# Kernel optimization log

Measured on AMD Instinct MI355X. Metric: run time of the kernel, lower is better.

## Reference

```python
import jax, jax.numpy as jnp
import numpy as np

N = 20000      # tuple-graph nodes
E = 320000     # edges per relation
F_IN = 5189    # 80 one-hot + 3*1703 node features
DIM = 256
N_ORIG = 183   # original texas graph nodes
C = 7


def _gcn(x, W, b, src, dst, n):
    # PyG GCNConv: add self loops, symmetric deg^-1/2 normalization, aggregate src->dst.
    loop = jnp.arange(n)
    s = jnp.concatenate([src, loop])
    d = jnp.concatenate([dst, loop])
    deg = jax.ops.segment_sum(jnp.ones(s.shape[0], x.dtype), d, num_segments=n)
    dinv = jnp.where(deg > 0, jax.lax.rsqrt(deg), 0.0)
    norm = dinv[s] * dinv[d]            # [E+n]
    h = x @ W                            # [n, dim]
    out = jax.ops.segment_sum(h[s] * norm[:, None], d, num_segments=n)
    return out + b


def _mlp(h, w1, b1, w2, b2):
    return jnp.maximum(h @ w1 + b1, 0.0) @ w2 + b2


def _seg_mean(h, idx, n):
    s = jax.ops.segment_sum(h, idx, num_segments=n)
    cnt = jax.ops.segment_sum(jnp.ones(idx.shape[0], h.dtype), idx, num_segments=n)
    return s / jnp.maximum(cnt, 1.0)[:, None]


def setup_inputs() -> dict:
    key = jax.random.key(0)
    ks = jax.random.split(key, 16)
    sc_in = 1.0 / np.sqrt(F_IN)
    sc_d = 1.0 / np.sqrt(DIM)
    sc_3d = 1.0 / np.sqrt(3 * DIM)
    inp = {
        'x': jax.random.normal(ks[0], (N, F_IN), jnp.float32),
        'w1': jax.random.normal(ks[1], (3, F_IN, DIM), jnp.float32) * sc_in,
        'b1': jnp.zeros((3, DIM), jnp.float32),
        'w2': jax.random.normal(ks[2], (3, DIM, DIM), jnp.float32) * sc_d,
        'b2': jnp.zeros((3, DIM), jnp.float32),
        'm1w1': jax.random.normal(ks[3], (3 * DIM, DIM), jnp.float32) * sc_3d,
        'm1b1': jnp.zeros((DIM,), jnp.float32),
        'm1w2': jax.random.normal(ks[4], (DIM, DIM), jnp.float32) * sc_d,
        'm1b2': jnp.zeros((DIM,), jnp.float32),
        'm2w1': jax.random.normal(ks[5], (3 * DIM, DIM), jnp.float32) * sc_3d,
        'm2b1': jnp.zeros((DIM,), jnp.float32),
        'm2w2': jax.random.normal(ks[6], (DIM, DIM), jnp.float32) * sc_d,
        'm2b2': jnp.zeros((DIM,), jnp.float32),
        'mw1': jax.random.normal(ks[7], (3 * DIM, DIM), jnp.float32) * sc_3d,
        'mb1': jnp.zeros((DIM,), jnp.float32),
        'mw2': jax.random.normal(ks[8], (DIM, C), jnp.float32) * sc_d,
        'mb2': jnp.zeros((C,), jnp.float32),
        'edge_index_1': jax.random.randint(ks[9], (2, E), 0, N),
        'edge_index_2': jax.random.randint(ks[10], (2, E), 0, N),
        'edge_index_3': jax.random.randint(ks[11], (2, E), 0, N),
        'index_1': jax.random.randint(ks[12], (N,), 0, N_ORIG),
        'index_2': jax.random.randint(ks[13], (N,), 0, N_ORIG),
        'index_3': jax.random.randint(ks[14], (N,), 0, N_ORIG),
    }
    return inp


def reference(x, w1, b1, w2, b2, m1w1, m1b1, m1w2, m1b2,
              m2w1, m2b1, m2w2, m2b2, mw1, mb1, mw2, mb2,
              edge_index_1, edge_index_2, edge_index_3,
              index_1, index_2, index_3):
    n = x.shape[0]
    eis = (edge_index_1, edge_index_2, edge_index_3)
    # layer 1: three GCN convs over the three relations, ReLU, concat, MLP
    hs = [jnp.maximum(_gcn(x, w1[i], b1[i], eis[i][0], eis[i][1], n), 0.0) for i in range(3)]
    h = _mlp(jnp.concatenate(hs, axis=-1), m1w1, m1b1, m1w2, m1b2)
    # layer 2
    hs = [jnp.maximum(_gcn(h, w2[i], b2[i], eis[i][0], eis[i][1], n), 0.0) for i in range(3)]
    h = _mlp(jnp.concatenate(hs, axis=-1), m2w1, m2b1, m2w2, m2b2)
    # faithful to source bug: index_2 is overwritten by index_3 before scatter
    x1 = _seg_mean(h, index_1, N_ORIG)
    x2 = _seg_mean(h, index_3, N_ORIG)
    x3 = _seg_mean(h, index_3, N_ORIG)
    out = _mlp(jnp.concatenate([x1, x2, x3], axis=1), mw1, mb1, mw2, mb2)
    return jax.nn.log_softmax(out, axis=1)
```

## Files before the change

### kernel.cpp

```cpp
#include <hip/hip_runtime.h>
#include <hip/hip_bf16.h>
#include <cstdint>
#include <cstddef>

typedef __bf16 bf16_t;
typedef __bf16 bf16x8 __attribute__((ext_vector_type(8)));
typedef float f32x4 __attribute__((ext_vector_type(4)));
typedef unsigned int u32x4 __attribute__((ext_vector_type(4)));

#define NN 20000
#define NE 320000
#define FIN 5189
#define KP1 5216
#define NORIG 183

__device__ inline f32x4 ld4u(const float* p) {
  f32x4 v; __builtin_memcpy(&v, p, 16); return v;
}

__device__ inline void gload_lds16(const bf16_t* g, bf16_t* l) {
  __builtin_amdgcn_global_load_lds(
      (const __attribute__((address_space(1))) uint32_t*)g,
      (__attribute__((address_space(3))) uint32_t*)l, 16, 0, 0);
}

__global__ void k_cvtpad(const float* __restrict__ x, bf16_t* __restrict__ xb) {
  const int total = NN * (KP1 / 8);
  for (int idx = blockIdx.x * 256 + threadIdx.x; idx < total; idx += gridDim.x * 256) {
    int row = idx / (KP1 / 8);
    int c8  = idx - row * (KP1 / 8);
    int col = c8 * 8;
    bf16x8 v{};
    const float* xp = x + (size_t)row * FIN + col;
    if (col + 8 <= FIN) {
      f32x4 a = ld4u(xp), b = ld4u(xp + 4);
#pragma unroll
      for (int j = 0; j < 4; ++j) { v[j] = (bf16_t)a[j]; v[4 + j] = (bf16_t)b[j]; }
    } else {
#pragma unroll
      for (int j = 0; j < 8; ++j) v[j] = (col + j < FIN) ? (bf16_t)xp[j] : (bf16_t)0.f;
    }
    *(bf16x8*)&xb[(size_t)row * KP1 + col] = v;
  }
}

#define BM1 128
#define BN1 256
#define NT1 (KP1 / 32)

__global__ __launch_bounds__(512) void k_gemm1(
    const bf16_t* __restrict__ A, const bf16_t* __restrict__ Bt,
    float* __restrict__ C, int M)
{
  __shared__ __align__(16) bf16_t As[2][BM1 * 32];
  __shared__ __align__(16) bf16_t Bs[2][BN1 * 32];
  const int tid = threadIdx.x, lane = tid & 63, wave = tid >> 6;
  const int m0 = blockIdx.y * BM1, n0 = blockIdx.x * BN1;
  const int wr = (wave >> 2) * 64, wc = (wave & 3) * 64;
  const int fm = lane & 15, fs = lane >> 4;

  const int arow = tid >> 2, asl = tid & 3;
  const int aks = asl ^ ((arow ^ (arow >> 2)) & 3);
  int agrow = m0 + arow; if (agrow >= M) agrow = M - 1;
  const bf16_t* asrc = A + (size_t)agrow * KP1 + aks * 8;

  const int br0 = tid >> 2;
  const int br1 = 128 + (tid >> 2);
  const int bks0 = asl ^ ((br0 ^ (br0 >> 2)) & 3);
  const int bks1 = asl ^ ((br1 ^ (br1 >> 2)) & 3);
  const bf16_t* bsrc0 = Bt + (size_t)(n0 + br0) * KP1 + bks0 * 8;
  const bf16_t* bsrc1 = Bt + (size_t)(n0 + br1) * KP1 + bks1 * 8;

  bf16_t* adst  = &As[0][0] + wave * 512;
  bf16_t* bdst0 = &Bs[0][0] + wave * 512;
  bf16_t* bdst1 = &Bs[0][0] + 4096 + wave * 512;

  int aoff[4], boff[4];
#pragma unroll
  for (int i = 0; i < 4; ++i) {
    int ra = wr + i * 16 + fm;
    aoff[i] = ra * 32 + ((fs ^ ((ra ^ (ra >> 2)) & 3)) * 8);
    int rb = wc + i * 16 + fm;
    boff[i] = rb * 32 + ((fs ^ ((rb ^ (rb >> 2)) & 3)) * 8);
  }

  f32x4 acc[4][4];
#pragma unroll
  for (int i = 0; i < 4; ++i)
#pragma unroll
    for (int j = 0; j < 4; ++j) acc[i][j] = {0.f, 0.f, 0.f, 0.f};

#define STAGE1(buf, kof) do { \
    gload_lds16(asrc + (kof),  adst  + (buf) * (BM1 * 32)); \
    gload_lds16(bsrc0 + (kof), bdst0 + (buf) * (BN1 * 32)); \
    gload_lds16(bsrc1 + (kof), bdst1 + (buf) * (BN1 * 32)); \
  } while (0)

  STAGE1(0, 0);
  __syncthreads();

  int buf = 0;
  for (int t = 0; t < NT1 - 1; ++t) {
    STAGE1(buf ^ 1, (t + 1) * 32);
    bf16x8 af[4], bfv[4];
#pragma unroll
    for (int i = 0; i < 4; ++i) af[i] = *(const bf16x8*)&As[buf][aoff[i]];
#pragma unroll
    for (int j = 0; j < 4; ++j) bfv[j] = *(const bf16x8*)&Bs[buf][boff[j]];
#pragma unroll
    for (int i = 0; i < 4; ++i)
#pragma unroll
      for (int j = 0; j < 4; ++j)
        acc[i][j] = __builtin_amdgcn_mfma_f32_16x16x32_bf16(af[i], bfv[j], acc[i][j], 0, 0, 0);
    __syncthreads();
    buf ^= 1;
  }
  {
    bf16x8 af[4], bfv[4];
#pragma unroll
    for (int i = 0; i < 4; ++i) af[i] = *(const bf16x8*)&As[buf][aoff[i]];
#pragma unroll
    for (int j = 0; j < 4; ++j) bfv[j] = *(const bf16x8*)&Bs[buf][boff[j]];
#pragma unroll
    for (int i = 0; i < 4; ++i)
#pragma unroll
      for (int j = 0; j < 4; ++j)
        acc[i][j] = __builtin_amdgcn_mfma_f32_16x16x32_bf16(af[i], bfv[j], acc[i][j], 0, 0, 0);
  }

  const int ccol = n0 + wc + fm;
#pragma unroll
  for (int i = 0; i < 4; ++i) {
    const int rb2 = m0 + wr + i * 16 + (lane >> 4) * 4;
#pragma unroll
    for (int r = 0; r < 4; ++r) {
      const int row = rb2 + r;
      if (row < M) {
        float* cp = C + (size_t)row * 768 + ccol;
#pragma unroll
        for (int j = 0; j < 4; ++j) cp[j * 16] = acc[i][j][r];
      }
    }
  }
}

#define BM 128
#define BN 128
#define BK 32
#define PADK 40

__global__ __launch_bounds__(256) void k_gemm(
    const float* __restrict__ A, const bf16_t* __restrict__ Bt,
    float* __restrict__ C, const float* __restrict__ bias,
    int M, int N, int K, int Kp, int relu)
{
  __shared__ __align__(16) bf16_t As[BM * PADK];
  __shared__ __align__(16) bf16_t Bs[BN * PADK];
  const int tid  = threadIdx.x;
  const int lane = tid & 63, wave = tid >> 6;
  const int m0 = blockIdx.y * BM, n0 = blockIdx.x * BN;
  const int wr = (wave >> 1) * 64, wc = (wave & 1) * 64;
  const int srow = tid >> 1;
  const int skh  = (tid & 1) * 16;
  const int arow = m0 + srow;
  const int fm = lane & 15;
  const int fk = (lane >> 4) * 8;

  f32x4 acc[4][4];
#pragma unroll
  for (int i = 0; i < 4; ++i)
#pragma unroll
    for (int j = 0; j < 4; ++j) acc[i][j] = {0.f, 0.f, 0.f, 0.f};

  for (int k0 = 0; k0 < Kp; k0 += BK) {
    {
      bf16x8 v0{}, v1{};
      if (arow < M) {
        const int kb = k0 + skh;
        const float* ap = A + (size_t)arow * K + kb;
        if (kb + 16 <= K) {
          f32x4 a = ld4u(ap), b = ld4u(ap + 4), c = ld4u(ap + 8), d = ld4u(ap + 12);
#pragma unroll
          for (int j = 0; j < 4; ++j) {
            v0[j]     = (bf16_t)a[j];
            v0[4 + j] = (bf16_t)b[j];
            v1[j]     = (bf16_t)c[j];
            v1[4 + j] = (bf16_t)d[j];
          }
        } else {
#pragma unroll
          for (int j = 0; j < 8; ++j) {
            int k1 = kb + j, k2 = kb + 8 + j;
            v0[j] = (bf16_t)((k1 < K) ? ap[j] : 0.f);
            v1[j] = (bf16_t)((k2 < K) ? ap[8 + j] : 0.f);
          }
        }
      }
      *(bf16x8*)&As[srow * PADK + skh]     = v0;
      *(bf16x8*)&As[srow * PADK + skh + 8] = v1;
    }
    {
      const bf16_t* bp = Bt + (size_t)(n0 + srow) * Kp + k0 + skh;
      u32x4 b0 = *(const u32x4*)bp;
      u32x4 b1 = *(const u32x4*)(bp + 8);
      *(u32x4*)&Bs[srow * PADK + skh]     = b0;
      *(u32x4*)&Bs[srow * PADK + skh + 8] = b1;
    }
    __syncthreads();

    bf16x8 af[4], bfv[4];
#pragma unroll
    for (int i = 0; i < 4; ++i) af[i] = *(const bf16x8*)&As[(wr + i * 16 + fm) * PADK + fk];
#pragma unroll
    for (int j = 0; j < 4; ++j) bfv[j] = *(const bf16x8*)&Bs[(wc + j * 16 + fm) * PADK + fk];
#pragma unroll
    for (int i = 0; i < 4; ++i)
#pragma unroll
      for (int j = 0; j < 4; ++j)
        acc[i][j] = __builtin_amdgcn_mfma_f32_16x16x32_bf16(af[i], bfv[j], acc[i][j], 0, 0, 0);
    __syncthreads();
  }

  const int ccol = n0 + wc + fm;
#pragma unroll
  for (int i = 0; i < 4; ++i) {
    const int rb = m0 + wr + i * 16 + (lane >> 4) * 4;
#pragma unroll
    for (int r = 0; r < 4; ++r) {
      const int row = rb + r;
      if (row < M) {
        float* cp = C + (size_t)row * N + ccol;
#pragma unroll
        for (int j = 0; j < 4; ++j) {
          float v = acc[i][j][r];
          if (bias) v += bias[ccol + j * 16];
          if (relu) v = fmaxf(v, 0.f);
          cp[j * 16] = v;
        }
      }
    }
  }
}

__global__ void k_transw(const float* __restrict__ src, bf16_t* __restrict__ dst,
                         int K, int Kp)
{
  __shared__ float tile[32][33];
  const int g = blockIdx.z;
  const int k0 = blockIdx.x * 32, j0 = blockIdx.y * 32;
  const int tx = threadIdx.x, ty = threadIdx.y;
  const float* sp = src + (size_t)g * K * 256;
#pragma unroll
  for (int i = 0; i < 4; ++i) {
    int k = k0 + ty + i * 8;
    tile[ty + i * 8][tx] = (k < K) ? sp[(size_t)k * 256 + j0 + tx] : 0.f;
  }
  __syncthreads();
  bf16_t* dp = dst + (size_t)g * 256 * Kp;
#pragma unroll
  for (int i = 0; i < 4; ++i) {
    int n = j0 + ty + i * 8;
    dp[(size_t)n * Kp + k0 + tx] = (bf16_t)tile[tx][ty + i * 8];
  }
}

__global__ void k_deg(const int* __restrict__ dst, int* __restrict__ cnt, int E) {
  int e = blockIdx.x * 256 + threadIdx.x;
  if (e < E) atomicAdd(&cnt[dst[e]], 1);
}

__global__ void k_dinv(const int* __restrict__ deg, float* __restrict__ dinv) {
  int v = blockIdx.x * 256 + threadIdx.x;
  if (v < 3 * NN) dinv[v] = rsqrtf((float)(deg[v] + 1));
}

#define SCAN_T 1024
#define SCAN_CH 20
__global__ __launch_bounds__(SCAN_T) void k_scan(
    const int* __restrict__ deg, int* __restrict__ rp, int* __restrict__ cur)
{
  const int r = blockIdx.x;
  const int* d = deg + r * NN;
  int* rpr = rp + r * (NN + 1);
  int* cr  = cur + r * NN;
  __shared__ int ts[SCAN_T];
  const int t = threadIdx.x;
  const int base = t * SCAN_CH;
  int local[SCAN_CH];
  int sum = 0;
#pragma unroll
  for (int i = 0; i < SCAN_CH; ++i) {
    int v = base + i;
    int x = (v < NN) ? d[v] : 0;
    local[i] = sum; sum += x;
  }
  ts[t] = sum; __syncthreads();
  for (int ofs = 1; ofs < SCAN_T; ofs <<= 1) {
    int v = ts[t];
    int w = (t >= ofs) ? ts[t - ofs] : 0;
    __syncthreads();
    ts[t] = v + w;
    __syncthreads();
  }
  int excl = (t == 0) ? 0 : ts[t - 1];
#pragma unroll
  for (int i = 0; i < SCAN_CH; ++i) {
    int v = base + i;
    if (v < NN) { int val = excl + local[i]; rpr[v] = val; cr[v] = val; }
  }
  if (t == SCAN_T - 1) rpr[NN] = ts[SCAN_T - 1];
}

__global__ void k_bucket(const int* __restrict__ src, const int* __restrict__ dst,
                         int* __restrict__ cur, int* __restrict__ col) {
  int e = blockIdx.x * 256 + threadIdx.x;
  if (e < NE) {
    int d = dst[e];
    int pos = atomicAdd(&cur[d], 1);
    col[pos] = src[e];
  }
}

__global__ __launch_bounds__(256) void k_gather(
    const float* __restrict__ H, float* __restrict__ Out,
    const int* __restrict__ rp, const int* __restrict__ col,
    const float* __restrict__ dinv, const float* __restrict__ bias)
{
  const int v = blockIdx.x, r = blockIdx.y, tid = threadIdx.x;
  const int roff = r << 8;
  const int* rpr = rp + r * (NN + 1);
  const int* cr  = col + (size_t)r * NE;
  const float* dvp = dinv + r * NN;
  const float dv = dvp[v];
  float acc = H[(size_t)v * 768 + roff + tid] * dv;
  int i = rpr[v];
  const int e = rpr[v + 1];
  for (; i + 4 <= e; i += 4) {
    int s0 = cr[i], s1 = cr[i + 1], s2 = cr[i + 2], s3 = cr[i + 3];
    float d0 = dvp[s0], d1 = dvp[s1], d2 = dvp[s2], d3 = dvp[s3];
    float h0 = H[(size_t)s0 * 768 + roff + tid];
    float h1 = H[(size_t)s1 * 768 + roff + tid];
    float h2 = H[(size_t)s2 * 768 + roff + tid];
    float h3 = H[(size_t)s3 * 768 + roff + tid];
    acc += h0 * d0 + h1 * d1 + h2 * d2 + h3 * d3;
  }
  for (; i < e; ++i) {
    int s = cr[i];
    acc += H[(size_t)s * 768 + roff + tid] * dvp[s];
  }
  Out[(size_t)v * 768 + roff + tid] = fmaxf(dv * acc + bias[roff + tid], 0.f);
}

__global__ void k_segscatter(const float* __restrict__ h2,
                             const int* __restrict__ i1, const int* __restrict__ i3,
                             float* __restrict__ s1, float* __restrict__ s3,
                             float* __restrict__ c1, float* __restrict__ c3) {
  int v = blockIdx.x, c = threadIdx.x;
  float val = h2[(size_t)v * 256 + c];
  int g1 = i1[v], g3 = i3[v];
  atomicAdd(&s1[g1 * 256 + c], val);
  atomicAdd(&s3[g3 * 256 + c], val);
  if (c == 0) { atomicAdd(&c1[g1], 1.f); atomicAdd(&c3[g3], 1.f); }
}

__global__ __launch_bounds__(256) void k_final(
    const float* __restrict__ s1, const float* __restrict__ s3,
    const float* __restrict__ c1, const float* __restrict__ c3,
    const float* __restrict__ mw1, const float* __restrict__ mb1,
    const float* __restrict__ mw2, const float* __restrict__ mb2,
    float* __restrict__ out)
{
  __shared__ float xc[768];
  __shared__ float tt[256];
  __shared__ float lg[8];
  const int g = blockIdx.x, tid = threadIdx.x;
  float inv1 = 1.f / fmaxf(c1[g], 1.f);
  float inv3 = 1.f / fmaxf(c3[g], 1.f);
  float a3 = s3[g * 256 + tid] * inv3;
  xc[tid] = s1[g * 256 + tid] * inv1;
  xc[256 + tid] = a3;
  xc[512 + tid] = a3;
  __syncthreads();
  float acc = mb1[tid];
  for (int k = 0; k < 768; ++k) acc += xc[k] * mw1[k * 256 + tid];
  tt[tid] = fmaxf(acc, 0.f);
  __syncthreads();
  if (tid < 7) {
    float a = mb2[tid];
    for (int k = 0; k < 256; ++k) a += tt[k] * mw2[k * 7 + tid];
    lg[tid] = a;
  }
  __syncthreads();
  if (tid == 0) {
    float mx = lg[0];
    for (int c2 = 1; c2 < 7; ++c2) mx = fmaxf(mx, lg[c2]);
    float sum = 0.f;
    for (int c2 = 0; c2 < 7; ++c2) sum += expf(lg[c2] - mx);
    float lse = logf(sum) + mx;
    for (int c2 = 0; c2 < 7; ++c2) out[g * 7 + c2] = lg[c2] - lse;
  }
}

extern "C" void kernel_launch(void* const* d_in, const int* in_sizes, int n_in,
                              void* d_out, int out_size, void* d_ws, size_t ws_size,
                              hipStream_t stream) {
  const float* x    = (const float*)d_in[0];
  const float* w1   = (const float*)d_in[1];
  const float* b1   = (const float*)d_in[2];
  const float* w2   = (const float*)d_in[3];
  const float* b2   = (const float*)d_in[4];
  const float* m1w1 = (const float*)d_in[5];
  const float* m1b1 = (const float*)d_in[6];
  const float* m1w2 = (const float*)d_in[7];
  const float* m1b2 = (const float*)d_in[8];
  const float* m2w1 = (const float*)d_in[9];
  const float* m2b1 = (const float*)d_in[10];
  const float* m2w2 = (const float*)d_in[11];
  const float* m2b2 = (const float*)d_in[12];
  const float* mw1  = (const float*)d_in[13];
  const float* mb1  = (const float*)d_in[14];
  const float* mw2  = (const float*)d_in[15];
  const float* mb2  = (const float*)d_in[16];
  const int* e1 = (const int*)d_in[17];
  const int* e2 = (const int*)d_in[18];
  const int* e3 = (const int*)d_in[19];
  const int* i1 = (const int*)d_in[20];
  const int* i3 = (const int*)d_in[22];
  float* out = (float*)d_out;

  char* ws = (char*)d_ws;
  size_t off = 0;
  auto alloc = [&](size_t bytes) {
    char* p = ws + off;
    off += (bytes + 255) & ~(size_t)255;
    return (void*)p;
  };
  float*  buf1 = (float*)alloc((size_t)NN * 768 * 4);
  float*  buf2 = (float*)alloc((size_t)NN * 768 * 4);
  bf16_t* wt   = (bf16_t*)alloc((size_t)768 * KP1 * 2);
  int*    deg  = (int*)alloc((size_t)3 * NN * 4);
  float*  dinv = (float*)alloc((size_t)3 * NN * 4);
  int*    rp   = (int*)alloc((size_t)3 * (NN + 1) * 4);
  int*    cur  = (int*)alloc((size_t)3 * NN * 4);
  int*    col  = (int*)alloc((size_t)3 * NE * 4);
  float*  s1   = (float*)alloc((size_t)NORIG * 256 * 4);
  float*  s3   = (float*)alloc((size_t)NORIG * 256 * 4);
  float*  c1   = (float*)alloc((size_t)NORIG * 4);
  float*  c3   = (float*)alloc((size_t)NORIG * 4);
  bf16_t* xb   = (bf16_t*)alloc((size_t)NN * KP1 * 2);
  const bool fast1 = (off <= ws_size);

  hipMemsetAsync(deg, 0, (size_t)3 * NN * 4, stream);
  int gb = (NE + 255) / 256;
  k_deg<<<gb, 256, 0, stream>>>(e1 + NE, deg + 0 * NN, NE);
  k_deg<<<gb, 256, 0, stream>>>(e2 + NE, deg + 1 * NN, NE);
  k_deg<<<gb, 256, 0, stream>>>(e3 + NE, deg + 2 * NN, NE);
  k_dinv<<<(3 * NN + 255) / 256, 256, 0, stream>>>(deg, dinv);
  k_scan<<<3, SCAN_T, 0, stream>>>(deg, rp, cur);
  k_bucket<<<gb, 256, 0, stream>>>(e1, e1 + NE, cur + 0 * NN, col + 0 * (size_t)NE);
  k_bucket<<<gb, 256, 0, stream>>>(e2, e2 + NE, cur + 1 * NN, col + 1 * (size_t)NE);
  k_bucket<<<gb, 256, 0, stream>>>(e3, e3 + NE, cur + 2 * NN, col + 2 * (size_t)NE);

  auto gemm = [&](const float* A, const float* Wsrc, int G, float* C, const float* bias,
                  int M, int N, int K, int relu) {
    int Kp = (K + 31) & ~31;
    dim3 tg(Kp / 32, 8, G);
    k_transw<<<tg, dim3(32, 8), 0, stream>>>(Wsrc, wt, K, Kp);
    dim3 gg(N / 128, (M + 127) / 128);
    k_gemm<<<gg, 256, 0, stream>>>(A, wt, C, bias, M, N, K, Kp, relu);
  };

  dim3 gagg(NN, 3);

  if (fast1) {
    k_transw<<<dim3(KP1 / 32, 8, 3), dim3(32, 8), 0, stream>>>(w1, wt, FIN, KP1);
    k_cvtpad<<<2048, 256, 0, stream>>>(x, xb);
    k_gemm1<<<dim3(768 / BN1, (NN + BM1 - 1) / BM1), 512, 0, stream>>>(xb, wt, buf1, NN);
  } else {
    gemm(x, w1, 3, buf1, nullptr, NN, 768, FIN, 0);
  }
  k_gather<<<gagg, 256, 0, stream>>>(buf1, buf2, rp, col, dinv, b1);
  gemm(buf2, m1w1, 1, buf1, m1b1, NN, 256, 768, 1);
  gemm(buf1, m1w2, 1, buf2, m1b2, NN, 256, 256, 0);

  gemm(buf2, w2, 3, buf1, nullptr, NN, 768, 256, 0);
  k_gather<<<gagg, 256, 0, stream>>>(buf1, buf2, rp, col, dinv, b2);
  gemm(buf2, m2w1, 1, buf1, m2b1, NN, 256, 768, 1);
  gemm(buf1, m2w2, 1, buf2, m2b2, NN, 256, 256, 0);

  hipMemsetAsync(s1, 0, (size_t)NORIG * 256 * 4, stream);
  hipMemsetAsync(s3, 0, (size_t)NORIG * 256 * 4, stream);
  hipMemsetAsync(c1, 0, (size_t)NORIG * 4, stream);
  hipMemsetAsync(c3, 0, (size_t)NORIG * 4, stream);
  k_segscatter<<<NN, 256, 0, stream>>>(buf2, i1, i3, s1, s3, c1, c3);
  k_final<<<NORIG, 256, 0, stream>>>(s1, s3, c1, c3, mw1, mb1, mw2, mb2, out);
}
```

Baseline: 1.073 ms.

## Store intermediate activations in bf16 and use async-LDS GEMMs throughout

```diff
diff --git a/kernel.cpp b/kernel.cpp
--- a/kernel.cpp
+++ b/kernel.cpp
@@ -5,8 +5,8 @@
 
 typedef __bf16 bf16_t;
 typedef __bf16 bf16x8 __attribute__((ext_vector_type(8)));
+typedef __bf16 bf16x4 __attribute__((ext_vector_type(4)));
 typedef float f32x4 __attribute__((ext_vector_type(4)));
-typedef unsigned int u32x4 __attribute__((ext_vector_type(4)));
 
 #define NN 20000
 #define NE 320000
@@ -23,6 +23,8 @@
       (const __attribute__((address_space(1))) uint32_t*)g,
       (__attribute__((address_space(3))) uint32_t*)l, 16, 0, 0);
 }
+
+__device__ inline int swz(int r) { return (r ^ (r >> 2)) & 3; }
 
 __global__ void k_cvtpad(const float* __restrict__ x, bf16_t* __restrict__ xb) {
   const int total = NN * (KP1 / 8);
@@ -44,32 +46,26 @@
   }
 }
 
-#define BM1 128
-#define BN1 256
-#define NT1 (KP1 / 32)
-
-__global__ __launch_bounds__(512) void k_gemm1(
+__global__ __launch_bounds__(512) void k_gemm_w(
     const bf16_t* __restrict__ A, const bf16_t* __restrict__ Bt,
-    float* __restrict__ C, int M)
+    bf16_t* __restrict__ C, const float* __restrict__ bias,
+    int M, int N, int Kp, int relu)
 {
-  __shared__ __align__(16) bf16_t As[2][BM1 * 32];
-  __shared__ __align__(16) bf16_t Bs[2][BN1 * 32];
+  __shared__ __align__(16) bf16_t As[2][128 * 32];
+  __shared__ __align__(16) bf16_t Bs[2][256 * 32];
   const int tid = threadIdx.x, lane = tid & 63, wave = tid >> 6;
-  const int m0 = blockIdx.y * BM1, n0 = blockIdx.x * BN1;
+  const int m0 = blockIdx.y * 128, n0 = blockIdx.x * 256;
   const int wr = (wave >> 2) * 64, wc = (wave & 3) * 64;
   const int fm = lane & 15, fs = lane >> 4;
 
   const int arow = tid >> 2, asl = tid & 3;
-  const int aks = asl ^ ((arow ^ (arow >> 2)) & 3);
+  const int aks = asl ^ swz(arow);
   int agrow = m0 + arow; if (agrow >= M) agrow = M - 1;
-  const bf16_t* asrc = A + (size_t)agrow * KP1 + aks * 8;
-
-  const int br0 = tid >> 2;
-  const int br1 = 128 + (tid >> 2);
-  const int bks0 = asl ^ ((br0 ^ (br0 >> 2)) & 3);
-  const int bks1 = asl ^ ((br1 ^ (br1 >> 2)) & 3);
-  const bf16_t* bsrc0 = Bt + (size_t)(n0 + br0) * KP1 + bks0 * 8;
-  const bf16_t* bsrc1 = Bt + (size_t)(n0 + br1) * KP1 + bks1 * 8;
+  const bf16_t* asrc = A + (size_t)agrow * Kp + aks * 8;
+
+  const int br0 = tid >> 2, br1 = 128 + br0;
+  const bf16_t* bsrc0 = Bt + (size_t)(n0 + br0) * Kp + (asl ^ swz(br0)) * 8;
+  const bf16_t* bsrc1 = Bt + (size_t)(n0 + br1) * Kp + (asl ^ swz(br1)) * 8;
 
   bf16_t* adst  = &As[0][0] + wave * 512;
   bf16_t* bdst0 = &Bs[0][0] + wave * 512;
@@ -79,9 +75,9 @@
 #pragma unroll
   for (int i = 0; i < 4; ++i) {
     int ra = wr + i * 16 + fm;
-    aoff[i] = ra * 32 + ((fs ^ ((ra ^ (ra >> 2)) & 3)) * 8);
+    aoff[i] = ra * 32 + (fs ^ swz(ra)) * 8;
     int rb = wc + i * 16 + fm;
-    boff[i] = rb * 32 + ((fs ^ ((rb ^ (rb >> 2)) & 3)) * 8);
+    boff[i] = rb * 32 + (fs ^ swz(rb)) * 8;
   }
 
   f32x4 acc[4][4];
@@ -90,18 +86,18 @@
 #pragma unroll
     for (int j = 0; j < 4; ++j) acc[i][j] = {0.f, 0.f, 0.f, 0.f};
 
-#define STAGE1(buf, kof) do { \
-    gload_lds16(asrc + (kof),  adst  + (buf) * (BM1 * 32)); \
-    gload_lds16(bsrc0 + (kof), bdst0 + (buf) * (BN1 * 32)); \
-    gload_lds16(bsrc1 + (kof), bdst1 + (buf) * (BN1 * 32)); \
+#define STAGEW(buf, kof) do { \
+    gload_lds16(asrc + (kof),  adst  + (buf) * (128 * 32)); \
+    gload_lds16(bsrc0 + (kof), bdst0 + (buf) * (256 * 32)); \
+    gload_lds16(bsrc1 + (kof), bdst1 + (buf) * (256 * 32)); \
   } while (0)
 
-  STAGE1(0, 0);
+  const int NT = Kp / 32;
+  STAGEW(0, 0);
   __syncthreads();
-
   int buf = 0;
-  for (int t = 0; t < NT1 - 1; ++t) {
-    STAGE1(buf ^ 1, (t + 1) * 32);
+  for (int t = 0; t < NT - 1; ++t) {
+    STAGEW(buf ^ 1, (t + 1) * 32);
     bf16x8 af[4], bfv[4];
 #pragma unroll
     for (int i = 0; i < 4; ++i) af[i] = *(const bf16x8*)&As[buf][aoff[i]];
@@ -136,106 +132,113 @@
     for (int r = 0; r < 4; ++r) {
       const int row = rb2 + r;
       if (row < M) {
-        float* cp = C + (size_t)row * 768 + ccol;
-#pragma unroll
-        for (int j = 0; j < 4; ++j) cp[j * 16] = acc[i][j][r];
-      }
-    }
-  }
-}
-
-#define BM 128
-#define BN 128
-#define BK 32
-#define PADK 40
-
-__global__ __launch_bounds__(256) void k_gemm(
-    const float* __restrict__ A, const bf16_t* __restrict__ Bt,
-    float* __restrict__ C, const float* __restrict__ bias,
-    int M, int N, int K, int Kp, int relu)
-{
-  __shared__ __align__(16) bf16_t As[BM * PADK];
-  __shared__ __align__(16) bf16_t Bs[BN * PADK];
-  const int tid  = threadIdx.x;
-  const int lane = tid & 63, wave = tid >> 6;
-  const int m0 = blockIdx.y * BM, n0 = blockIdx.x * BN;
-  const int wr = (wave >> 1) * 64, wc = (wave & 1) * 64;
-  const int srow = tid >> 1;
-  const int skh  = (tid & 1) * 16;
-  const int arow = m0 + srow;
-  const int fm = lane & 15;
-  const int fk = (lane >> 4) * 8;
-
-  f32x4 acc[4][4];
-#pragma unroll
-  for (int i = 0; i < 4; ++i)
-#pragma unroll
-    for (int j = 0; j < 4; ++j) acc[i][j] = {0.f, 0.f, 0.f, 0.f};
-
-  for (int k0 = 0; k0 < Kp; k0 += BK) {
-    {
-      bf16x8 v0{}, v1{};
-      if (arow < M) {
-        const int kb = k0 + skh;
-        const float* ap = A + (size_t)arow * K + kb;
-        if (kb + 16 <= K) {
-          f32x4 a = ld4u(ap), b = ld4u(ap + 4), c = ld4u(ap + 8), d = ld4u(ap + 12);
-#pragma unroll
-          for (int j = 0; j < 4; ++j) {
-            v0[j]     = (bf16_t)a[j];
-            v0[4 + j] = (bf16_t)b[j];
-            v1[j]     = (bf16_t)c[j];
-            v1[4 + j] = (bf16_t)d[j];
-          }
-        } else {
-#pragma unroll
-          for (int j = 0; j < 8; ++j) {
-            int k1 = kb + j, k2 = kb + 8 + j;
-            v0[j] = (bf16_t)((k1 < K) ? ap[j] : 0.f);
-            v1[j] = (bf16_t)((k2 < K) ? ap[8 + j] : 0.f);
-          }
-        }
-      }
-      *(bf16x8*)&As[srow * PADK + skh]     = v0;
-      *(bf16x8*)&As[srow * PADK + skh + 8] = v1;
-    }
-    {
-      const bf16_t* bp = Bt + (size_t)(n0 + srow) * Kp + k0 + skh;
-      u32x4 b0 = *(const u32x4*)bp;
-      u32x4 b1 = *(const u32x4*)(bp + 8);
-      *(u32x4*)&Bs[srow * PADK + skh]     = b0;
-      *(u32x4*)&Bs[srow * PADK + skh + 8] = b1;
-    }
-    __syncthreads();
-
-    bf16x8 af[4], bfv[4];
-#pragma unroll
-    for (int i = 0; i < 4; ++i) af[i] = *(const bf16x8*)&As[(wr + i * 16 + fm) * PADK + fk];
-#pragma unroll
-    for (int j = 0; j < 4; ++j) bfv[j] = *(const bf16x8*)&Bs[(wc + j * 16 + fm) * PADK + fk];
-#pragma unroll
-    for (int i = 0; i < 4; ++i)
-#pragma unroll
-      for (int j = 0; j < 4; ++j)
-        acc[i][j] = __builtin_amdgcn_mfma_f32_16x16x32_bf16(af[i], bfv[j], acc[i][j], 0, 0, 0);
-    __syncthreads();
-  }
-
-  const int ccol = n0 + wc + fm;
-#pragma unroll
-  for (int i = 0; i < 4; ++i) {
-    const int rb = m0 + wr + i * 16 + (lane >> 4) * 4;
-#pragma unroll
-    for (int r = 0; r < 4; ++r) {
-      const int row = rb + r;
-      if (row < M) {
-        float* cp = C + (size_t)row * N + ccol;
+        bf16_t* cp = C + (size_t)row * N + ccol;
 #pragma unroll
         for (int j = 0; j < 4; ++j) {
           float v = acc[i][j][r];
           if (bias) v += bias[ccol + j * 16];
           if (relu) v = fmaxf(v, 0.f);
-          cp[j * 16] = v;
+          cp[j * 16] = (bf16_t)v;
+        }
+      }
+    }
+  }
+}
+
+__global__ __launch_bounds__(256) void k_gemm_s(
+    const bf16_t* __restrict__ A, const bf16_t* __restrict__ Bt,
+    bf16_t* __restrict__ C, const float* __restrict__ bias,
+    int M, int N, int Kp, int relu)
+{
+  __shared__ __align__(16) bf16_t As[2][128 * 32];
+  __shared__ __align__(16) bf16_t Bs[2][128 * 32];
+  const int tid = threadIdx.x, lane = tid & 63, wave = tid >> 6;
+  const int m0 = blockIdx.y * 128, n0 = blockIdx.x * 128;
+  const int wr = (wave >> 1) * 64, wc = (wave & 1) * 64;
+  const int fm = lane & 15, fs = lane >> 4;
+
+  const int r0 = tid >> 2, r1 = 64 + r0, sl = tid & 3;
+  int ag0 = m0 + r0; if (ag0 >= M) ag0 = M - 1;
+  int ag1 = m0 + r1; if (ag1 >= M) ag1 = M - 1;
+  const bf16_t* asrc0 = A + (size_t)ag0 * Kp + (sl ^ swz(r0)) * 8;
+  const bf16_t* asrc1 = A + (size_t)ag1 * Kp + (sl ^ swz(r1)) * 8;
+  const bf16_t* bsrc0 = Bt + (size_t)(n0 + r0) * Kp + (sl ^ swz(r0)) * 8;
+  const bf16_t* bsrc1 = Bt + (size_t)(n0 + r1) * Kp + (sl ^ swz(r1)) * 8;
+
+  bf16_t* adst0 = &As[0][0] + wave * 512;
+  bf16_t* adst1 = &As[0][0] + 2048 + wave * 512;
+  bf16_t* bdst0 = &Bs[0][0] + wave * 512;
+  bf16_t* bdst1 = &Bs[0][0] + 2048 + wave * 512;
+
+  int aoff[4], boff[4];
+#pragma unroll
+  for (int i = 0; i < 4; ++i) {
+    int ra = wr + i * 16 + fm;
+    aoff[i] = ra * 32 + (fs ^ swz(ra)) * 8;
+    int rb = wc + i * 16 + fm;
+    boff[i] = rb * 32 + (fs ^ swz(rb)) * 8;
+  }
+
+  f32x4 acc[4][4];
+#pragma unroll
+  for (int i = 0; i < 4; ++i)
+#pragma unroll
+    for (int j = 0; j < 4; ++j) acc[i][j] = {0.f, 0.f, 0.f, 0.f};
+
+#define STAGES(buf, kof) do { \
+    gload_lds16(asrc0 + (kof), adst0 + (buf) * (128 * 32)); \
+    gload_lds16(asrc1 + (kof), adst1 + (buf) * (128 * 32)); \
+    gload_lds16(bsrc0 + (kof), bdst0 + (buf) * (128 * 32)); \
+    gload_lds16(bsrc1 + (kof), bdst1 + (buf) * (128 * 32)); \
+  } while (0)
+
+  const int NT = Kp / 32;
+  STAGES(0, 0);
+  __syncthreads();
+  int buf = 0;
+  for (int t = 0; t < NT - 1; ++t) {
+    STAGES(buf ^ 1, (t + 1) * 32);
+    bf16x8 af[4], bfv[4];
+#pragma unroll
+    for (int i = 0; i < 4; ++i) af[i] = *(const bf16x8*)&As[buf][aoff[i]];
+#pragma unroll
+    for (int j = 0; j < 4; ++j) bfv[j] = *(const bf16x8*)&Bs[buf][boff[j]];
+#pragma unroll
+    for (int i = 0; i < 4; ++i)
+#pragma unroll
+      for (int j = 0; j < 4; ++j)
+        acc[i][j] = __builtin_amdgcn_mfma_f32_16x16x32_bf16(af[i], bfv[j], acc[i][j], 0, 0, 0);
+    __syncthreads();
+    buf ^= 1;
+  }
+  {
+    bf16x8 af[4], bfv[4];
+#pragma unroll
+    for (int i = 0; i < 4; ++i) af[i] = *(const bf16x8*)&As[buf][aoff[i]];
+#pragma unroll
+    for (int j = 0; j < 4; ++j) bfv[j] = *(const bf16x8*)&Bs[buf][boff[j]];
+#pragma unroll
+    for (int i = 0; i < 4; ++i)
+#pragma unroll
+      for (int j = 0; j < 4; ++j)
+        acc[i][j] = __builtin_amdgcn_mfma_f32_16x16x32_bf16(af[i], bfv[j], acc[i][j], 0, 0, 0);
+  }
+
+  const int ccol = n0 + wc + fm;
+#pragma unroll
+  for (int i = 0; i < 4; ++i) {
+    const int rb2 = m0 + wr + i * 16 + (lane >> 4) * 4;
+#pragma unroll
+    for (int r = 0; r < 4; ++r) {
+      const int row = rb2 + r;
+      if (row < M) {
+        bf16_t* cp = C + (size_t)row * N + ccol;
+#pragma unroll
+        for (int j = 0; j < 4; ++j) {
+          float v = acc[i][j][r];
+          if (bias) v += bias[ccol + j * 16];
+          if (relu) v = fmaxf(v, 0.f);
+          cp[j * 16] = (bf16_t)v;
         }
       }
     }
@@ -321,42 +324,59 @@
   }
 }
 
-__global__ __launch_bounds__(256) void k_gather(
-    const float* __restrict__ H, float* __restrict__ Out,
+__global__ __launch_bounds__(256) void k_gatherb(
+    const bf16_t* __restrict__ H, bf16_t* __restrict__ Out,
     const int* __restrict__ rp, const int* __restrict__ col,
     const float* __restrict__ dinv, const float* __restrict__ bias)
 {
-  const int v = blockIdx.x, r = blockIdx.y, tid = threadIdx.x;
+  const int wv = threadIdx.x >> 6, lane = threadIdx.x & 63;
+  const int v = blockIdx.x * 4 + wv;
+  const int r = blockIdx.y;
   const int roff = r << 8;
   const int* rpr = rp + r * (NN + 1);
   const int* cr  = col + (size_t)r * NE;
   const float* dvp = dinv + r * NN;
   const float dv = dvp[v];
-  float acc = H[(size_t)v * 768 + roff + tid] * dv;
+  const int c0 = roff + lane * 4;
+
+  bf16x4 hs = *(const bf16x4*)&H[(size_t)v * 768 + c0];
+  float a0 = (float)hs[0] * dv, a1 = (float)hs[1] * dv,
+        a2 = (float)hs[2] * dv, a3 = (float)hs[3] * dv;
+
   int i = rpr[v];
   const int e = rpr[v + 1];
-  for (; i + 4 <= e; i += 4) {
-    int s0 = cr[i], s1 = cr[i + 1], s2 = cr[i + 2], s3 = cr[i + 3];
-    float d0 = dvp[s0], d1 = dvp[s1], d2 = dvp[s2], d3 = dvp[s3];
-    float h0 = H[(size_t)s0 * 768 + roff + tid];
-    float h1 = H[(size_t)s1 * 768 + roff + tid];
-    float h2 = H[(size_t)s2 * 768 + roff + tid];
-    float h3 = H[(size_t)s3 * 768 + roff + tid];
-    acc += h0 * d0 + h1 * d1 + h2 * d2 + h3 * d3;
-  }
-  for (; i < e; ++i) {
+  for (; i + 2 <= e; i += 2) {
+    int s0 = cr[i], s1 = cr[i + 1];
+    float d0 = dvp[s0], d1 = dvp[s1];
+    bf16x4 h0 = *(const bf16x4*)&H[(size_t)s0 * 768 + c0];
+    bf16x4 h1 = *(const bf16x4*)&H[(size_t)s1 * 768 + c0];
+    a0 += (float)h0[0] * d0 + (float)h1[0] * d1;
+    a1 += (float)h0[1] * d0 + (float)h1[1] * d1;
+    a2 += (float)h0[2] * d0 + (float)h1[2] * d1;
+    a3 += (float)h0[3] * d0 + (float)h1[3] * d1;
+  }
+  if (i < e) {
     int s = cr[i];
-    acc += H[(size_t)s * 768 + roff + tid] * dvp[s];
-  }
-  Out[(size_t)v * 768 + roff + tid] = fmaxf(dv * acc + bias[roff + tid], 0.f);
-}
-
-__global__ void k_segscatter(const float* __restrict__ h2,
+    float d = dvp[s];
+    bf16x4 h = *(const bf16x4*)&H[(size_t)s * 768 + c0];
+    a0 += (float)h[0] * d; a1 += (float)h[1] * d;
+    a2 += (float)h[2] * d; a3 += (float)h[3] * d;
+  }
+  f32x4 bb = ld4u(bias + c0);
+  bf16x4 o;
+  o[0] = (bf16_t)fmaxf(dv * a0 + bb[0], 0.f);
+  o[1] = (bf16_t)fmaxf(dv * a1 + bb[1], 0.f);
+  o[2] = (bf16_t)fmaxf(dv * a2 + bb[2], 0.f);
+  o[3] = (bf16_t)fmaxf(dv * a3 + bb[3], 0.f);
+  *(bf16x4*)&Out[(size_t)v * 768 + c0] = o;
+}
+
+__global__ void k_segscatter(const bf16_t* __restrict__ h2,
                              const int* __restrict__ i1, const int* __restrict__ i3,
                              float* __restrict__ s1, float* __restrict__ s3,
                              float* __restrict__ c1, float* __restrict__ c3) {
   int v = blockIdx.x, c = threadIdx.x;
-  float val = h2[(size_t)v * 256 + c];
+  float val = (float)h2[(size_t)v * 256 + c];
   int g1 = i1[v], g3 = i3[v];
   atomicAdd(&s1[g1 * 256 + c], val);
   atomicAdd(&s3[g3 * 256 + c], val);
@@ -435,9 +455,12 @@
     off += (bytes + 255) & ~(size_t)255;
     return (void*)p;
   };
-  float*  buf1 = (float*)alloc((size_t)NN * 768 * 4);
-  float*  buf2 = (float*)alloc((size_t)NN * 768 * 4);
+  bf16_t* xb   = (bf16_t*)alloc((size_t)NN * KP1 * 2);
   bf16_t* wt   = (bf16_t*)alloc((size_t)768 * KP1 * 2);
+  bf16_t* a1   = (bf16_t*)alloc((size_t)NN * 768 * 2);
+  bf16_t* g1   = (bf16_t*)alloc((size_t)NN * 768 * 2);
+  bf16_t* t1   = (bf16_t*)alloc((size_t)NN * 256 * 2);
+  bf16_t* h1   = (bf16_t*)alloc((size_t)NN * 256 * 2);
   int*    deg  = (int*)alloc((size_t)3 * NN * 4);
   float*  dinv = (float*)alloc((size_t)3 * NN * 4);
   int*    rp   = (int*)alloc((size_t)3 * (NN + 1) * 4);
@@ -447,8 +470,6 @@
   float*  s3   = (float*)alloc((size_t)NORIG * 256 * 4);
   float*  c1   = (float*)alloc((size_t)NORIG * 4);
   float*  c3   = (float*)alloc((size_t)NORIG * 4);
-  bf16_t* xb   = (bf16_t*)alloc((size_t)NN * KP1 * 2);
-  const bool fast1 = (off <= ws_size);
 
   hipMemsetAsync(deg, 0, (size_t)3 * NN * 4, stream);
   int gb = (NE + 255) / 256;
@@ -461,37 +482,33 @@
   k_bucket<<<gb, 256, 0, stream>>>(e2, e2 + NE, cur + 1 * NN, col + 1 * (size_t)NE);
   k_bucket<<<gb, 256, 0, stream>>>(e3, e3 + NE, cur + 2 * NN, col + 2 * (size_t)NE);
 
-  auto gemm = [&](const float* A, const float* Wsrc, int G, float* C, const float* bias,
-                  int M, int N, int K, int relu) {
-    int Kp = (K + 31) & ~31;
-    dim3 tg(Kp / 32, 8, G);
-    k_transw<<<tg, dim3(32, 8), 0, stream>>>(Wsrc, wt, K, Kp);
-    dim3 gg(N / 128, (M + 127) / 128);
-    k_gemm<<<gg, 256, 0, stream>>>(A, wt, C, bias, M, N, K, Kp, relu);
+  auto transw = [&](const float* Wsrc, int G, int K, int Kp) {
+    k_transw<<<dim3(Kp / 32, 8, G), dim3(32, 8), 0, stream>>>(Wsrc, wt, K, Kp);
   };
 
-  dim3 gagg(NN, 3);
-
-  if (fast1) {
-    k_transw<<<dim3(KP1 / 32, 8, 3), dim3(32, 8), 0, stream>>>(w1, wt, FIN, KP1);
-    k_cvtpad<<<2048, 256, 0, stream>>>(x, xb);
-    k_gemm1<<<dim3(768 / BN1, (NN + BM1 - 1) / BM1), 512, 0, stream>>>(xb, wt, buf1, NN);
-  } else {
-    gemm(x, w1, 3, buf1, nullptr, NN, 768, FIN, 0);
-  }
-  k_gather<<<gagg, 256, 0, stream>>>(buf1, buf2, rp, col, dinv, b1);
-  gemm(buf2, m1w1, 1, buf1, m1b1, NN, 256, 768, 1);
-  gemm(buf1, m1w2, 1, buf2, m1b2, NN, 256, 256, 0);
-
-  gemm(buf2, w2, 3, buf1, nullptr, NN, 768, 256, 0);
-  k_gather<<<gagg, 256, 0, stream>>>(buf1, buf2, rp, col, dinv, b2);
-  gemm(buf2, m2w1, 1, buf1, m2b1, NN, 256, 768, 1);
-  gemm(buf1, m2w2, 1, buf2, m2b2, NN, 256, 256, 0);
+  dim3 ggat(NN / 4, 3);
+
+  transw(w1, 3, FIN, KP1);
+  k_cvtpad<<<2048, 256, 0, stream>>>(x, xb);
+  k_gemm_w<<<dim3(3, 157), 512, 0, stream>>>(xb, wt, a1, nullptr, NN, 768, KP1, 0);
+  k_gatherb<<<ggat, 256, 0, stream>>>(a1, g1, rp, col, dinv, b1);
+  transw(m1w1, 1, 768, 768);
+  k_gemm_s<<<dim3(2, 157), 256, 0, stream>>>(g1, wt, t1, m1b1, NN, 256, 768, 1);
+  transw(m1w2, 1, 256, 256);
+  k_gemm_s<<<dim3(2, 157), 256, 0, stream>>>(t1, wt, h1, m1b2, NN, 256, 256, 0);
+
+  transw(w2, 3, 256, 256);
+  k_gemm_w<<<dim3(3, 157), 512, 0, stream>>>(h1, wt, a1, nullptr, NN, 768, 256, 0);
+  k_gatherb<<<ggat, 256, 0, stream>>>(a1, g1, rp, col, dinv, b2);
+  transw(m2w1, 1, 768, 768);
+  k_gemm_s<<<dim3(2, 157), 256, 0, stream>>>(g1, wt, t1, m2b1, NN, 256, 768, 1);
+  transw(m2w2, 1, 256, 256);
+  k_gemm_s<<<dim3(2, 157), 256, 0, stream>>>(t1, wt, h1, m2b2, NN, 256, 256, 0);
 
   hipMemsetAsync(s1, 0, (size_t)NORIG * 256 * 4, stream);
   hipMemsetAsync(s3, 0, (size_t)NORIG * 256 * 4, stream);
   hipMemsetAsync(c1, 0, (size_t)NORIG * 4, stream);
   hipMemsetAsync(c3, 0, (size_t)NORIG * 4, stream);
-  k_segscatter<<<NN, 256, 0, stream>>>(buf2, i1, i3, s1, s3, c1, c3);
+  k_segscatter<<<NN, 256, 0, stream>>>(h1, i1, i3, s1, s3, c1, c3);
   k_final<<<NORIG, 256, 0, stream>>>(s1, s3, c1, c3, mw1, mb1, mw2, mb2, out);
 }
```

Result: faster. 898.9 us (-16.2%).
